# Kernel optimization log

Hardware: AMD Instinct MI355X
Metric: run time of the kernel (lower is better)

Reference implementation:

```python
import jax, jax.numpy as jnp
import numpy as np

EPS = 1e-20

def _log(t):
    return jnp.log(jnp.clip(t, EPS, None))

def setup_inputs() -> dict:
    key = jax.random.key(0)
    k1, k2 = jax.random.split(key)
    L, B, D = 1, 8192, 128
    a = jax.random.normal(k1, (L, B, D), dtype=jnp.float32)
    t = jax.random.normal(k2, (L, B, D), dtype=jnp.float32)
    # latents are L2-normalized (standard practice before this contrastive loss;
    # keeps exp(temp * sim) finite with init_temp=10)
    a = a / jnp.linalg.norm(a, axis=-1, keepdims=True)
    t = t / jnp.linalg.norm(t, axis=-1, keepdims=True)
    temperatures = jnp.full((1, 1, 1), np.log(10.0), dtype=jnp.float32)
    return {"audio_latents": a, "text_latents": t, "temperatures": temperatures}

def reference(audio_latents, text_latents, temperatures):
    # audio_latents, text_latents: (L, B, D); single-process so all_gather is identity
    L, B, D = audio_latents.shape
    N = L * B
    a = audio_latents.reshape(N, D)
    t = text_latents.reshape(N, D)
    # sims: (N, N); layers=1 so temperatures.exp() is a scalar broadcast
    sims = jnp.einsum('id,jd->ij', a, t) * jnp.exp(temperatures[0, 0, 0])
    exp_sims = jnp.exp(sims)
    numerator = jnp.diagonal(exp_sims)  # (N,)
    # decoupled contrastive learning: zero the diagonal before the denominators
    idx = jnp.arange(N)
    exp_masked = exp_sims.at[idx, idx].set(0.0)
    den_i = jnp.sum(exp_masked, axis=1)  # row sums (N,)
    den_j = jnp.sum(exp_masked, axis=0)  # col sums (N,)
    loss = -_log(numerator) + 0.5 * (_log(den_i) + _log(den_j))
    return jnp.mean(loss).reshape(1)  # matches reduce('1 n -> 1', 'mean')
```

## Files before the change

kernel.cpp:

```cpp
#include <hip/hip_runtime.h>
#include <hip/hip_bf16.h>


typedef __attribute__((ext_vector_type(8))) int   v8i;
typedef __attribute__((ext_vector_type(4))) float f32x4;

#define SCALE_ONE 0x7F7F7F7F

__device__ __forceinline__ float fast_exp2(float x) {
#if __has_builtin(__builtin_amdgcn_exp2f)
    return __builtin_amdgcn_exp2f(x);
#else
    return __expf(x * 0.69314718056f);
#endif
}

template <int CTRL>
__device__ __forceinline__ float dpp_sr_add(float v) {
    int s = __builtin_amdgcn_update_dpp(0, __float_as_int(v), CTRL, 0xf, 0xf, true);
    return v + __int_as_float(s);
}
__device__ __forceinline__ float row16_sum(float v) {
    v = dpp_sr_add<0x111>(v);
    v = dpp_sr_add<0x112>(v);
    v = dpp_sr_add<0x114>(v);
    v = dpp_sr_add<0x118>(v);
    return v;
}

__global__ void convert_pack(const float* __restrict__ a,
                             const float* __restrict__ t,
                             const float* __restrict__ temps,
                             unsigned char* __restrict__ oa,
                             unsigned char* __restrict__ ot) {
    int idx = blockIdx.x * 256 + threadIdx.x;
    const bool isT = (idx >> 16) != 0;
    const float* src = isT ? t : a;
    unsigned char* dst = isT ? ot : oa;
    const float s = isT ? 1.0f : (__expf(temps[0]) * 1.44269504f);
    int loc = idx & 65535;
    int tile = loc >> 7, sub = loc & 127;
    int lane = sub >> 1, h = sub & 1;
    int row = tile * 16 + (lane & 15);
    int k0  = (lane >> 4) * 32 + h * 16;
    const float4* s4 = reinterpret_cast<const float4*>(src + row * 128 + k0);
    unsigned w[4];
#pragma unroll
    for (int q = 0; q < 4; ++q) {
        float4 f = s4[q];
        int v = __builtin_amdgcn_cvt_pk_fp8_f32(f.x * s, f.y * s, 0, false);
        v = __builtin_amdgcn_cvt_pk_fp8_f32(f.z * s, f.w * s, v, true);
        w[q] = (unsigned)v;
    }
    *reinterpret_cast<uint4*>(dst + tile * 2048 + lane * 32 + h * 16) =
        make_uint4(w[0], w[1], w[2], w[3]);
}

#define PHASE(BF, COLBASE)                                              \
  {                                                                     \
    f32x4 acc[4][2];                                                    \
    _Pragma("unroll") for (int m = 0; m < 4; ++m)                       \
      _Pragma("unroll") for (int n = 0; n < 2; ++n)                     \
        acc[m][n] = (f32x4){0.f, 0.f, 0.f, 0.f};                        \
    _Pragma("unroll") for (int m = 0; m < 4; ++m)                       \
      _Pragma("unroll") for (int n = 0; n < 2; ++n)                     \
        acc[m][n] = __builtin_amdgcn_mfma_scale_f32_16x16x128_f8f6f4(   \
            af[m], BF[n], acc[m][n], 0, 0, 0, SCALE_ONE, 0, SCALE_ONE); \
    float csum[2] = {0.f, 0.f};                                         \
    _Pragma("unroll") for (int m = 0; m < 4; ++m)                       \
      _Pragma("unroll") for (int n = 0; n < 2; ++n)                     \
        _Pragma("unroll") for (int jj = 0; jj < 4; ++jj) {              \
          float v = fast_exp2(acc[m][n][jj]);                           \
          rsum[m][jj] += v;                                             \
          csum[n] += v;                                                 \
        }                                                               \
    _Pragma("unroll") for (int n = 0; n < 2; ++n) {                     \
      float v = csum[n];                                                \
      v += __shfl_xor(v, 16); v += __shfl_xor(v, 32);                   \
      if (lane < 16) {                                                  \
        int col = (COLBASE + n) * 16 + lcol;                            \
        Pj[col * 128 + rs] = v;                                         \
      }                                                                 \
    }                                                                   \
  }

__global__ void __launch_bounds__(256)
gemm_exp(const unsigned char* __restrict__ Ap, const unsigned char* __restrict__ Tp,
         float* __restrict__ Pi, float* __restrict__ Pj) {
    const int tid = threadIdx.x;
    const int wave = tid >> 6, lane = tid & 63;
    const int krow = lane >> 4, lcol = lane & 15;
    const int fid = blockIdx.x;
    const int vid = (fid & 7) * 128 + (fid >> 3);
    const int j  = vid >> 5;
    const int rg = vid & 31;
    const int rs = rg * 4 + wave;

    v8i af[4];
#pragma unroll
    for (int m = 0; m < 4; ++m)
        af[m] = *reinterpret_cast<const v8i*>(Ap + (rs * 4 + m) * 2048 + lane * 32);

    const unsigned char* tb = Tp + j * 16 * 2048 + lane * 32;

    float rsum[4][4] = {};
    v8i bfA[2], bfB[2];

    bfA[0] = *reinterpret_cast<const v8i*>(tb);
    bfA[1] = *reinterpret_cast<const v8i*>(tb + 2048);

#pragma unroll 1
    for (int ph2 = 0; ph2 < 4; ++ph2) {
        const unsigned char* base = tb + ph2 * 8192;

        bfB[0] = *reinterpret_cast<const v8i*>(base + 2 * 2048);
        bfB[1] = *reinterpret_cast<const v8i*>(base + 3 * 2048);

        PHASE(bfA, j * 16 + ph2 * 4);

        if (ph2 < 3) {
            bfA[0] = *reinterpret_cast<const v8i*>(base + 8192);
            bfA[1] = *reinterpret_cast<const v8i*>(base + 8192 + 2048);
        }

        PHASE(bfB, j * 16 + ph2 * 4 + 2);
    }

#pragma unroll
    for (int m = 0; m < 4; ++m)
#pragma unroll
        for (int jj = 0; jj < 4; ++jj) {
            float v = row16_sum(rsum[m][jj]);
            if (lcol == 15) {
                int row = rs * 64 + m * 16 + krow * 4 + jj;
                Pi[row * 32 + j] = v;
            }
        }
}

__global__ void finalize_rows(const float* __restrict__ a, const float* __restrict__ t,
                              const float* __restrict__ temps,
                              const float* __restrict__ Pi, const float* __restrict__ Pj,
                              float* __restrict__ loss) {
    const int r = blockIdx.x * 4 + (threadIdx.x >> 6);
    const int l = threadIdx.x & 63;
    const float sc = __expf(temps[0]);
    float deni = (l < 32) ? Pi[r * 32 + l] : 0.f;
    float denj = Pj[r * 128 + l] + Pj[r * 128 + 64 + l];
    float dotp = a[r * 128 + l] * t[r * 128 + l]
               + a[r * 128 + 64 + l] * t[r * 128 + 64 + l];
#pragma unroll
    for (int m = 1; m < 64; m <<= 1) {
        deni += __shfl_xor(deni, m);
        denj += __shfl_xor(denj, m);
        dotp += __shfl_xor(dotp, m);
    }
    if (l == 0) {
        float diag = __expf(sc * dotp);
        float di = fmaxf(deni - diag, 1e-20f);
        float dj = fmaxf(denj - diag, 1e-20f);
        loss[r] = -sc * dotp + 0.5f * (__logf(di) + __logf(dj));
    }
}

__global__ void reduce_loss(const float* __restrict__ loss, float* __restrict__ out) {
    __shared__ float wsum[16];
    const int tid = threadIdx.x;
    float s = 0.f;
#pragma unroll
    for (int i = 0; i < 8; ++i) s += loss[tid + i * 1024];
#pragma unroll
    for (int m = 1; m < 64; m <<= 1) s += __shfl_xor(s, m);
    if ((tid & 63) == 0) wsum[tid >> 6] = s;
    __syncthreads();
    if (tid == 0) {
        float acc = 0.f;
#pragma unroll
        for (int w = 0; w < 16; ++w) acc += wsum[w];
        out[0] = acc * (1.0f / 8192.0f);
    }
}

extern "C" void kernel_launch(void* const* d_in, const int* in_sizes, int n_in,
                              void* d_out, int out_size, void* d_ws, size_t ws_size,
                              hipStream_t stream) {
    const float* a     = (const float*)d_in[0];
    const float* t     = (const float*)d_in[1];
    const float* temps = (const float*)d_in[2];
    float* out = (float*)d_out;

    char* ws = (char*)d_ws;
    unsigned char* Ap = (unsigned char*)(ws);
    unsigned char* Tp = (unsigned char*)(ws + (1u << 20));
    float* Pi  = (float*)(ws + (2u << 20));
    float* Pj  = (float*)(ws + (4u << 20));
    float* los = (float*)(ws + (8u << 20));

    convert_pack<<<512, 256, 0, stream>>>(a, t, temps, Ap, Tp);
    gemm_exp<<<1024, 256, 0, stream>>>(Ap, Tp, Pi, Pj);
    finalize_rows<<<2048, 256, 0, stream>>>(a, t, temps, Pi, Pj, los);
    reduce_loss<<<1, 1024, 0, stream>>>(los, out);
}
```

Baseline: 34.33 us.

## Fully unroll GEMM loop, defer column-sum shuffles, fuse final reduction via atomic counter

The gemm_exp phase loop is fully unrolled with explicit double-buffered B loads. Column partial sums are kept in registers and written out after all phases, which moves the cross-lane shuffles and global stores out of the MFMA/exp loop. The separate reduce_loss kernel is merged into the finalize kernel using a last-block-done atomic counter, removing one launch at the cost of a memset and atomics. The fully unrolled code holds more live registers, which may raise register pressure.

```diff
diff --git a/kernel.cpp b/kernel.cpp
--- a/kernel.cpp
+++ b/kernel.cpp
@@ -56,32 +56,33 @@
         make_uint4(w[0], w[1], w[2], w[3]);
 }
 
-#define PHASE(BF, COLBASE)                                              \
-  {                                                                     \
-    f32x4 acc[4][2];                                                    \
-    _Pragma("unroll") for (int m = 0; m < 4; ++m)                       \
-      _Pragma("unroll") for (int n = 0; n < 2; ++n)                     \
-        acc[m][n] = (f32x4){0.f, 0.f, 0.f, 0.f};                        \
-    _Pragma("unroll") for (int m = 0; m < 4; ++m)                       \
-      _Pragma("unroll") for (int n = 0; n < 2; ++n)                     \
-        acc[m][n] = __builtin_amdgcn_mfma_scale_f32_16x16x128_f8f6f4(   \
-            af[m], BF[n], acc[m][n], 0, 0, 0, SCALE_ONE, 0, SCALE_ONE); \
-    float csum[2] = {0.f, 0.f};                                         \
-    _Pragma("unroll") for (int m = 0; m < 4; ++m)                       \
-      _Pragma("unroll") for (int n = 0; n < 2; ++n)                     \
-        _Pragma("unroll") for (int jj = 0; jj < 4; ++jj) {              \
-          float v = fast_exp2(acc[m][n][jj]);                           \
-          rsum[m][jj] += v;                                             \
-          csum[n] += v;                                                 \
-        }                                                               \
-    _Pragma("unroll") for (int n = 0; n < 2; ++n) {                     \
-      float v = csum[n];                                                \
-      v += __shfl_xor(v, 16); v += __shfl_xor(v, 32);                   \
-      if (lane < 16) {                                                  \
-        int col = (COLBASE + n) * 16 + lcol;                            \
-        Pj[col * 128 + rs] = v;                                         \
-      }                                                                 \
-    }                                                                   \
+#define LD2(BUF, T0)                                                     \
+    BUF[0] = *reinterpret_cast<const v8i*>(tb + (T0) * 2048);            \
+    BUF[1] = *reinterpret_cast<const v8i*>(tb + (T0 + 1) * 2048);
+
+#define PHASE(BF, C0)                                                    \
+  {                                                                      \
+    f32x4 acc[4][2];                                                     \
+    _Pragma("unroll") for (int m = 0; m < 4; ++m)                        \
+      _Pragma("unroll") for (int n = 0; n < 2; ++n)                      \
+        acc[m][n] = (f32x4){0.f, 0.f, 0.f, 0.f};                         \
+    _Pragma("unroll") for (int m = 0; m < 4; ++m)                        \
+      _Pragma("unroll") for (int n = 0; n < 2; ++n)                      \
+        acc[m][n] = __builtin_amdgcn_mfma_scale_f32_16x16x128_f8f6f4(    \
+            af[m], BF[n], acc[m][n], 0, 0, 0, SCALE_ONE, 0, SCALE_ONE);  \
+    _Pragma("unroll") for (int n = 0; n < 2; ++n) {                      \
+      float cm[4];                                                       \
+      _Pragma("unroll") for (int m = 0; m < 4; ++m) {                    \
+        float v0 = fast_exp2(acc[m][n][0]);                              \
+        float v1 = fast_exp2(acc[m][n][1]);                              \
+        float v2 = fast_exp2(acc[m][n][2]);                              \
+        float v3 = fast_exp2(acc[m][n][3]);                              \
+        rsum[m][0] += v0; rsum[m][1] += v1;                              \
+        rsum[m][2] += v2; rsum[m][3] += v3;                              \
+        cm[m] = (v0 + v1) + (v2 + v3);                                   \
+      }                                                                  \
+      cs[(C0) + n] = (cm[0] + cm[1]) + (cm[2] + cm[3]);                  \
+    }                                                                    \
   }
 
 __global__ void __launch_bounds__(256)
@@ -104,26 +105,34 @@
     const unsigned char* tb = Tp + j * 16 * 2048 + lane * 32;
 
     float rsum[4][4] = {};
+    float cs[16];
     v8i bfA[2], bfB[2];
 
-    bfA[0] = *reinterpret_cast<const v8i*>(tb);
-    bfA[1] = *reinterpret_cast<const v8i*>(tb + 2048);
-
-#pragma unroll 1
-    for (int ph2 = 0; ph2 < 4; ++ph2) {
-        const unsigned char* base = tb + ph2 * 8192;
-
-        bfB[0] = *reinterpret_cast<const v8i*>(base + 2 * 2048);
-        bfB[1] = *reinterpret_cast<const v8i*>(base + 3 * 2048);
-
-        PHASE(bfA, j * 16 + ph2 * 4);
-
-        if (ph2 < 3) {
-            bfA[0] = *reinterpret_cast<const v8i*>(base + 8192);
-            bfA[1] = *reinterpret_cast<const v8i*>(base + 8192 + 2048);
+    LD2(bfA, 0)
+    LD2(bfB, 2)
+    PHASE(bfA, 0)
+    LD2(bfA, 4)
+    PHASE(bfB, 2)
+    LD2(bfB, 6)
+    PHASE(bfA, 4)
+    LD2(bfA, 8)
+    PHASE(bfB, 6)
+    LD2(bfB, 10)
+    PHASE(bfA, 8)
+    LD2(bfA, 12)
+    PHASE(bfB, 10)
+    LD2(bfB, 14)
+    PHASE(bfA, 12)
+    PHASE(bfB, 14)
+
+#pragma unroll
+    for (int c = 0; c < 16; ++c) {
+        float v = cs[c];
+        v += __shfl_xor(v, 16); v += __shfl_xor(v, 32);
+        if (lane < 16) {
+            int col = (j * 16 + c) * 16 + lcol;
+            Pj[col * 128 + rs] = v;
         }
-
-        PHASE(bfB, j * 16 + ph2 * 4 + 2);
     }
 
 #pragma unroll
@@ -138,12 +147,13 @@
         }
 }
 
-__global__ void finalize_rows(const float* __restrict__ a, const float* __restrict__ t,
-                              const float* __restrict__ temps,
-                              const float* __restrict__ Pi, const float* __restrict__ Pj,
-                              float* __restrict__ loss) {
-    const int r = blockIdx.x * 4 + (threadIdx.x >> 6);
-    const int l = threadIdx.x & 63;
+__global__ void finalize_fused(const float* __restrict__ a, const float* __restrict__ t,
+                               const float* __restrict__ temps,
+                               const float* __restrict__ Pi, const float* __restrict__ Pj,
+                               float* __restrict__ partial, int* __restrict__ counter,
+                               float* __restrict__ out) {
+    const int wave = threadIdx.x >> 6, l = threadIdx.x & 63;
+    const int r = blockIdx.x * 4 + wave;
     const float sc = __expf(temps[0]);
     float deni = (l < 32) ? Pi[r * 32 + l] : 0.f;
     float denj = Pj[r * 128 + l] + Pj[r * 128 + 64 + l];
@@ -155,29 +165,37 @@
         denj += __shfl_xor(denj, m);
         dotp += __shfl_xor(dotp, m);
     }
+    __shared__ float ls[4];
+    __shared__ int isLast;
     if (l == 0) {
         float diag = __expf(sc * dotp);
         float di = fmaxf(deni - diag, 1e-20f);
         float dj = fmaxf(denj - diag, 1e-20f);
-        loss[r] = -sc * dotp + 0.5f * (__logf(di) + __logf(dj));
-    }
-}
-
-__global__ void reduce_loss(const float* __restrict__ loss, float* __restrict__ out) {
-    __shared__ float wsum[16];
-    const int tid = threadIdx.x;
-    float s = 0.f;
-#pragma unroll
-    for (int i = 0; i < 8; ++i) s += loss[tid + i * 1024];
-#pragma unroll
-    for (int m = 1; m < 64; m <<= 1) s += __shfl_xor(s, m);
-    if ((tid & 63) == 0) wsum[tid >> 6] = s;
+        ls[wave] = -sc * dotp + 0.5f * (__logf(di) + __logf(dj));
+    }
     __syncthreads();
-    if (tid == 0) {
-        float acc = 0.f;
-#pragma unroll
-        for (int w = 0; w < 16; ++w) acc += wsum[w];
-        out[0] = acc * (1.0f / 8192.0f);
+    if (threadIdx.x == 0) {
+        float p = (ls[0] + ls[1]) + (ls[2] + ls[3]);
+        __hip_atomic_store(&partial[blockIdx.x], p, __ATOMIC_RELEASE,
+                           __HIP_MEMORY_SCOPE_AGENT);
+        int old = __hip_atomic_fetch_add(counter, 1, __ATOMIC_ACQ_REL,
+                                         __HIP_MEMORY_SCOPE_AGENT);
+        isLast = (old == (int)gridDim.x - 1);
+    }
+    __syncthreads();
+    if (isLast) {
+        float s = 0.f;
+#pragma unroll
+        for (int i = 0; i < 8; ++i)
+            s += __hip_atomic_load(&partial[threadIdx.x + i * 256],
+                                   __ATOMIC_RELAXED, __HIP_MEMORY_SCOPE_AGENT);
+#pragma unroll
+        for (int m = 1; m < 64; m <<= 1) s += __shfl_xor(s, m);
+        __shared__ float wsum[4];
+        if (l == 0) wsum[wave] = s;
+        __syncthreads();
+        if (threadIdx.x == 0)
+            out[0] = ((wsum[0] + wsum[1]) + (wsum[2] + wsum[3])) * (1.0f / 8192.0f);
     }
 }
 
@@ -192,12 +210,13 @@
     char* ws = (char*)d_ws;
     unsigned char* Ap = (unsigned char*)(ws);
     unsigned char* Tp = (unsigned char*)(ws + (1u << 20));
-    float* Pi  = (float*)(ws + (2u << 20));
-    float* Pj  = (float*)(ws + (4u << 20));
-    float* los = (float*)(ws + (8u << 20));
-
+    float* Pi      = (float*)(ws + (2u << 20));
+    float* Pj      = (float*)(ws + (4u << 20));
+    float* partial = (float*)(ws + (8u << 20));
+    int*   counter = (int*)(ws + (8u << 20) + 8192);
+
+    hipMemsetAsync(counter, 0, sizeof(int), stream);
     convert_pack<<<512, 256, 0, stream>>>(a, t, temps, Ap, Tp);
     gemm_exp<<<1024, 256, 0, stream>>>(Ap, Tp, Pi, Pj);
-    finalize_rows<<<2048, 256, 0, stream>>>(a, t, temps, Pi, Pj, los);
-    reduce_loss<<<1, 1024, 0, stream>>>(los, out);
-}
+    finalize_fused<<<2048, 256, 0, stream>>>(a, t, temps, Pi, Pj, partial, counter, out);
+}
```

Measured after the change: 103.5 us. +201.4%, slower.

## Stage shared text tiles in LDS via async global-to-LDS loads

Applied to the files above, without the earlier changes.

The block's 16 text tiles (32KB) are now loaded once into shared memory with global_load_lds, split across the four waves, instead of each wave reading them from global memory separately. The text pack layout is changed so each tile is stored as two contiguous 1KB halves that match the 16-byte direct-to-LDS loads. The phase loop is fully unrolled, with B fragments read from LDS ahead of each phase. This cuts redundant global and L2 traffic but adds a block-wide barrier and 32KB of LDS per block, which may lower occupancy.

```diff
diff --git a/kernel.cpp b/kernel.cpp
--- a/kernel.cpp
+++ b/kernel.cpp
@@ -3,9 +3,14 @@
 
 
 typedef __attribute__((ext_vector_type(8))) int   v8i;
+typedef __attribute__((ext_vector_type(4))) int   v4i;
 typedef __attribute__((ext_vector_type(4))) float f32x4;
 
 #define SCALE_ONE 0x7F7F7F7F
+
+#define GLD16(g, l) __builtin_amdgcn_global_load_lds(                         \
+    (const __attribute__((address_space(1))) unsigned int*)(const void*)(g),  \
+    (__attribute__((address_space(3))) unsigned int*)(void*)(l), 16, 0, 0)
 
 __device__ __forceinline__ float fast_exp2(float x) {
 #if __has_builtin(__builtin_amdgcn_exp2f)
@@ -52,41 +57,56 @@
         v = __builtin_amdgcn_cvt_pk_fp8_f32(f.z * s, f.w * s, v, true);
         w[q] = (unsigned)v;
     }
-    *reinterpret_cast<uint4*>(dst + tile * 2048 + lane * 32 + h * 16) =
-        make_uint4(w[0], w[1], w[2], w[3]);
-}
-
-#define PHASE(BF, COLBASE)                                              \
-  {                                                                     \
-    f32x4 acc[4][2];                                                    \
-    _Pragma("unroll") for (int m = 0; m < 4; ++m)                       \
-      _Pragma("unroll") for (int n = 0; n < 2; ++n)                     \
-        acc[m][n] = (f32x4){0.f, 0.f, 0.f, 0.f};                        \
-    _Pragma("unroll") for (int m = 0; m < 4; ++m)                       \
-      _Pragma("unroll") for (int n = 0; n < 2; ++n)                     \
-        acc[m][n] = __builtin_amdgcn_mfma_scale_f32_16x16x128_f8f6f4(   \
-            af[m], BF[n], acc[m][n], 0, 0, 0, SCALE_ONE, 0, SCALE_ONE); \
-    float csum[2] = {0.f, 0.f};                                         \
-    _Pragma("unroll") for (int m = 0; m < 4; ++m)                       \
-      _Pragma("unroll") for (int n = 0; n < 2; ++n)                     \
-        _Pragma("unroll") for (int jj = 0; jj < 4; ++jj) {              \
-          float v = fast_exp2(acc[m][n][jj]);                           \
-          rsum[m][jj] += v;                                             \
-          csum[n] += v;                                                 \
-        }                                                               \
-    _Pragma("unroll") for (int n = 0; n < 2; ++n) {                     \
-      float v = csum[n];                                                \
-      v += __shfl_xor(v, 16); v += __shfl_xor(v, 32);                   \
-      if (lane < 16) {                                                  \
-        int col = (COLBASE + n) * 16 + lcol;                            \
-        Pj[col * 128 + rs] = v;                                         \
-      }                                                                 \
-    }                                                                   \
+    int off = isT ? (tile * 2048 + h * 1024 + lane * 16)
+                  : (tile * 2048 + lane * 32 + h * 16);
+    *reinterpret_cast<uint4*>(dst + off) = make_uint4(w[0], w[1], w[2], w[3]);
+}
+
+__device__ __forceinline__ v8i ld_tile(const unsigned char* lds, int tile, int lane) {
+    v4i lo = *reinterpret_cast<const v4i*>(lds + tile * 2048 + lane * 16);
+    v4i hi = *reinterpret_cast<const v4i*>(lds + tile * 2048 + 1024 + lane * 16);
+    v8i r;
+    r[0] = lo[0]; r[1] = lo[1]; r[2] = lo[2]; r[3] = lo[3];
+    r[4] = hi[0]; r[5] = hi[1]; r[6] = hi[2]; r[7] = hi[3];
+    return r;
+}
+
+#define LD2(BUF, T0)                                                     \
+    BUF[0] = ld_tile(ldsT, (T0), lane);                                  \
+    BUF[1] = ld_tile(ldsT, (T0) + 1, lane);
+
+#define PHASE(BF, COLBASE)                                               \
+  {                                                                      \
+    f32x4 acc[4][2];                                                     \
+    _Pragma("unroll") for (int m = 0; m < 4; ++m)                        \
+      _Pragma("unroll") for (int n = 0; n < 2; ++n)                      \
+        acc[m][n] = (f32x4){0.f, 0.f, 0.f, 0.f};                         \
+    _Pragma("unroll") for (int m = 0; m < 4; ++m)                        \
+      _Pragma("unroll") for (int n = 0; n < 2; ++n)                      \
+        acc[m][n] = __builtin_amdgcn_mfma_scale_f32_16x16x128_f8f6f4(    \
+            af[m], BF[n], acc[m][n], 0, 0, 0, SCALE_ONE, 0, SCALE_ONE);  \
+    float csum[2] = {0.f, 0.f};                                          \
+    _Pragma("unroll") for (int m = 0; m < 4; ++m)                        \
+      _Pragma("unroll") for (int n = 0; n < 2; ++n)                      \
+        _Pragma("unroll") for (int jj = 0; jj < 4; ++jj) {               \
+          float v = fast_exp2(acc[m][n][jj]);                            \
+          rsum[m][jj] += v;                                              \
+          csum[n] += v;                                                  \
+        }                                                                \
+    _Pragma("unroll") for (int n = 0; n < 2; ++n) {                      \
+      float v = csum[n];                                                 \
+      v += __shfl_xor(v, 16); v += __shfl_xor(v, 32);                    \
+      if (lane < 16) {                                                   \
+        int col = (COLBASE + n) * 16 + lcol;                             \
+        Pj[col * 128 + rs] = v;                                          \
+      }                                                                  \
+    }                                                                    \
   }
 
 __global__ void __launch_bounds__(256)
 gemm_exp(const unsigned char* __restrict__ Ap, const unsigned char* __restrict__ Tp,
          float* __restrict__ Pi, float* __restrict__ Pj) {
+    __shared__ unsigned char ldsT[32768];
     const int tid = threadIdx.x;
     const int wave = tid >> 6, lane = tid & 63;
     const int krow = lane >> 4, lcol = lane & 15;
@@ -96,35 +116,40 @@
     const int rg = vid & 31;
     const int rs = rg * 4 + wave;
 
+    const unsigned char* gT = Tp + j * 16 * 2048;
+#pragma unroll
+    for (int tt = 0; tt < 4; ++tt) {
+        int tile = wave * 4 + tt;
+        GLD16(gT + tile * 2048 + lane * 16,        &ldsT[tile * 2048]);
+        GLD16(gT + tile * 2048 + 1024 + lane * 16, &ldsT[tile * 2048 + 1024]);
+    }
+
     v8i af[4];
 #pragma unroll
     for (int m = 0; m < 4; ++m)
         af[m] = *reinterpret_cast<const v8i*>(Ap + (rs * 4 + m) * 2048 + lane * 32);
 
-    const unsigned char* tb = Tp + j * 16 * 2048 + lane * 32;
+    __syncthreads();
 
     float rsum[4][4] = {};
     v8i bfA[2], bfB[2];
 
-    bfA[0] = *reinterpret_cast<const v8i*>(tb);
-    bfA[1] = *reinterpret_cast<const v8i*>(tb + 2048);
-
-#pragma unroll 1
-    for (int ph2 = 0; ph2 < 4; ++ph2) {
-        const unsigned char* base = tb + ph2 * 8192;
-
-        bfB[0] = *reinterpret_cast<const v8i*>(base + 2 * 2048);
-        bfB[1] = *reinterpret_cast<const v8i*>(base + 3 * 2048);
-
-        PHASE(bfA, j * 16 + ph2 * 4);
-
-        if (ph2 < 3) {
-            bfA[0] = *reinterpret_cast<const v8i*>(base + 8192);
-            bfA[1] = *reinterpret_cast<const v8i*>(base + 8192 + 2048);
-        }
-
-        PHASE(bfB, j * 16 + ph2 * 4 + 2);
-    }
+    LD2(bfA, 0)
+    LD2(bfB, 2)
+    PHASE(bfA, j * 16 + 0)
+    LD2(bfA, 4)
+    PHASE(bfB, j * 16 + 2)
+    LD2(bfB, 6)
+    PHASE(bfA, j * 16 + 4)
+    LD2(bfA, 8)
+    PHASE(bfB, j * 16 + 6)
+    LD2(bfB, 10)
+    PHASE(bfA, j * 16 + 8)
+    LD2(bfA, 12)
+    PHASE(bfB, j * 16 + 10)
+    LD2(bfB, 14)
+    PHASE(bfA, j * 16 + 12)
+    PHASE(bfB, j * 16 + 14)
 
 #pragma unroll
     for (int m = 0; m < 4; ++m)
```

Result: slower. 42.14 us (+22.8%).
